# Kernel optimization log

Hardware: AMD Instinct MI355X
Metric: run time of the kernel (lower is better)

## Reference

```python
import math
import jax, jax.numpy as jnp
import numpy as np

DIM = 512; DEPTH = 12; HEADS = 8; DIM_HEAD = 64
INNER = HEADS * DIM_HEAD
FF_INNER = 4 * DIM
B = 8192
NUM_TIMESTEPS = 1000
SCALE = 16.0  # cosine_sim_scale
ROT_DIM = 32  # RotaryEmbedding(dim=min(32, dim_head))
NUM_BUCKETS = 32; MAX_DISTANCE = 128


def layer_norm(x, g, eps=1e-5):
    mean = jnp.mean(x, axis=-1, keepdims=True)
    var = jnp.mean((x - mean) ** 2, axis=-1, keepdims=True)  # unbiased=False
    return (x - mean) * jax.lax.rsqrt(var + eps) * g


def l2norm(t):
    n = jnp.linalg.norm(t, axis=-1, keepdims=True)
    return t / jnp.maximum(n, 1e-12)


def rotary_freqs(n):
    inv = 1.0 / (10000.0 ** (jnp.arange(0, ROT_DIM, 2, dtype=jnp.float32) / ROT_DIM))
    f = jnp.arange(n, dtype=jnp.float32)[:, None] * inv[None, :]  # (n, ROT_DIM//2)
    return jnp.repeat(f, 2, axis=-1)  # (n, ROT_DIM), interleaved pairs


def rotate_half(x):
    x1 = x[..., 0::2]; x2 = x[..., 1::2]
    return jnp.stack((-x2, x1), axis=-1).reshape(x.shape)


def apply_rotary(t, freqs):
    tr, tp = t[..., :ROT_DIM], t[..., ROT_DIM:]
    tr = tr * jnp.cos(freqs) + rotate_half(tr) * jnp.sin(freqs)
    return jnp.concatenate([tr, tp], axis=-1)


def rel_pos_bias(i, j, emb):
    rel = jnp.arange(j)[None, :] - jnp.arange(i)[:, None]
    n = jnp.maximum(-rel, 0)
    max_exact = NUM_BUCKETS // 2
    nf = jnp.maximum(n, 1).astype(jnp.float32)
    val_large = max_exact + (jnp.log(nf / max_exact) / math.log(MAX_DISTANCE / max_exact) * (NUM_BUCKETS - max_exact)).astype(jnp.int32)
    val_large = jnp.minimum(val_large, NUM_BUCKETS - 1)
    bucket = jnp.where(n < max_exact, n, val_large)
    return emb[bucket].transpose(2, 0, 1)  # (h, i, j)


def setup_inputs() -> dict:
    key = jax.random.key(0)
    ks = jax.random.split(key, 13)
    w = 0.02
    return {
        "image_embed": jax.random.normal(ks[0], (B, DIM), jnp.float32),
        "text_embed": jax.random.normal(ks[1], (B, DIM), jnp.float32),
        "timesteps": jax.random.randint(ks[2], (B,), 0, NUM_TIMESTEPS),
        "time_emb_table": jax.random.normal(ks[3], (NUM_TIMESTEPS, DIM)) * w,
        "learned_query": jax.random.normal(ks[4], (DIM,)),
        "rel_emb": jax.random.normal(ks[5], (NUM_BUCKETS, HEADS)) * w,
        "attn_norm_g": jnp.ones((DEPTH, DIM)),
        "Wq": jax.random.normal(ks[6], (DEPTH, DIM, INNER)) * w,
        "Wkv": jax.random.normal(ks[7], (DEPTH, DIM, 2 * DIM_HEAD)) * w,
        "null_kv": jax.random.normal(ks[8], (DEPTH, 2, DIM_HEAD)),
        "Wo": jax.random.normal(ks[9], (DEPTH, INNER, DIM)) * w,
        "attn_out_norm_g": jnp.ones((DEPTH, DIM)),
        "ff_norm_g": jnp.ones((DEPTH, DIM)),
        "Wff1": jax.random.normal(ks[10], (DEPTH, DIM, 2 * FF_INNER)) * w,
        "Wff2": jax.random.normal(ks[11], (DEPTH, FF_INNER, DIM)) * w,
        "final_norm_g": jnp.ones((DIM,)),
        "Wproj": jax.random.normal(ks[12], (DIM, DIM)) * w,
    }


def reference(image_embed, text_embed, timesteps, time_emb_table, learned_query, rel_emb,
              attn_norm_g, Wq, Wkv, null_kv, Wo, attn_out_norm_g,
              ff_norm_g, Wff1, Wff2, final_norm_g, Wproj):
    b = image_embed.shape[0]
    # token sequence: [text_embed, time_embed, image_embed, learned_query] -> (b, 4, dim)
    tokens = jnp.concatenate([
        text_embed[:, None, :],
        time_emb_table[timesteps][:, None, :],
        image_embed[:, None, :],
        jnp.broadcast_to(learned_query, (b, 1, DIM)),
    ], axis=1)
    n = tokens.shape[1]
    bias = rel_pos_bias(n, n + 1, rel_emb)            # (h, n, n+1)
    freqs = rotary_freqs(n)                           # (n, ROT_DIM)
    causal = jnp.triu(jnp.ones((n, n + 1), dtype=bool), k=2)
    neg = -jnp.finfo(jnp.float32).max
    sqrt_scale = math.sqrt(SCALE)

    x = tokens
    for l in range(DEPTH):
        # --- Attention ---
        h = layer_norm(x, attn_norm_g[l])
        q = (h @ Wq[l]).reshape(b, n, HEADS, DIM_HEAD).transpose(0, 2, 1, 3) * SCALE
        kv = h @ Wkv[l]
        k, v = kv[..., :DIM_HEAD], kv[..., DIM_HEAD:]  # single-head kv (b, n, d)
        q = apply_rotary(q, freqs)
        k = apply_rotary(k, freqs)
        nk = jnp.broadcast_to(null_kv[l, 0], (b, 1, DIM_HEAD))
        nv = jnp.broadcast_to(null_kv[l, 1], (b, 1, DIM_HEAD))
        k = jnp.concatenate([nk, k], axis=1)
        v = jnp.concatenate([nv, v], axis=1)
        q = l2norm(q) * sqrt_scale
        k = l2norm(k) * sqrt_scale
        sim = jnp.einsum('bhid,bjd->bhij', q, k) + bias[None]
        sim = jnp.where(causal[None, None], neg, sim)
        attn = jax.nn.softmax(sim.astype(jnp.float32), axis=-1).astype(sim.dtype)
        out = jnp.einsum('bhij,bjd->bhid', attn, v).transpose(0, 2, 1, 3).reshape(b, n, INNER)
        x = x + layer_norm(out @ Wo[l], attn_out_norm_g[l])
        # --- SwiGLU FFN ---
        h = layer_norm(x, ff_norm_g[l])
        hg = h @ Wff1[l]
        a, g = hg[..., :FF_INNER], hg[..., FF_INNER:]
        x = x + (a * jax.nn.silu(g)) @ Wff2[l]

    x = layer_norm(x, final_norm_g) @ Wproj
    return x[:, -1, :]  # predicted image embed from learned query position
```

## Files before the change

### kernel.cpp

```cpp
#include <hip/hip_runtime.h>

typedef __bf16 bf16x8 __attribute__((ext_vector_type(8)));
typedef __bf16 bf16x4 __attribute__((ext_vector_type(4)));
typedef __bf16 bf16x2 __attribute__((ext_vector_type(2)));
typedef float  f32x4  __attribute__((ext_vector_type(4)));
typedef unsigned short u16;

#define BATCH   8192
#define NTOK    4
#define ROWS    (BATCH*NTOK)
#define DIM     512
#define HEADS   8
#define DH      64
#define FFI     2048
#define DEPTH   12
#define LN_EPS  1e-5f

static const size_t OFF_WQKV = 0;
static const size_t SZ_WQKV  = 12ull*640*512*2;
static const size_t OFF_WTO  = OFF_WQKV + SZ_WQKV;
static const size_t SZ_WTO   = 12ull*512*512*2;
static const size_t OFF_WTF1 = OFF_WTO + SZ_WTO;
static const size_t SZ_WTF1  = 12ull*4096*512*2;
static const size_t OFF_WTF2 = OFF_WTF1 + SZ_WTF1;
static const size_t SZ_WTF2  = 12ull*512*2048*2;
static const size_t OFF_WTP  = OFF_WTF2 + SZ_WTF2;
static const size_t SZ_WTP   = 512ull*512*2;
static const size_t OFF_X    = OFF_WTP + SZ_WTP;
static const size_t OFF_H    = OFF_X    + (size_t)ROWS*DIM*4;
static const size_t OFF_QKV  = OFF_H    + (size_t)ROWS*DIM*2;
static const size_t OFF_AO   = OFF_QKV  + (size_t)ROWS*640*2;
static const size_t OFF_FLAG = OFF_AO   + (size_t)ROWS*DIM*2;
static const size_t WS_NEED  = OFF_FLAG + 256;

__device__ __forceinline__ float ldf(const void* p, size_t i, bool b16) {
  return b16 ? (float)((const __bf16*)p)[i] : ((const float*)p)[i];
}

__device__ __forceinline__ void gld_lds16(const void* g, void* l) {
  __builtin_amdgcn_global_load_lds((const __attribute__((address_space(1))) void*)g,
                                   (__attribute__((address_space(3))) void*)l, 16, 0, 0);
}

__device__ __forceinline__ float gsum16(float v) {
  #pragma unroll
  for (int o = 8; o > 0; o >>= 1) v += __shfl_xor(v, o, 64);
  return v;
}

__device__ __forceinline__ void wred2(float& a, float& b) {
  #pragma unroll
  for (int o = 32; o > 0; o >>= 1) { a += __shfl_xor(a, o, 64); b += __shfl_xor(b, o, 64); }
}

__global__ void detect_dtype(const unsigned int* __restrict__ w, int* __restrict__ flag) {
  __shared__ int cnt[4];
  int t = threadIdx.x;
  int c = 0;
  for (int i = t; i < 2048; i += 256) {
    unsigned int v = w[i];
    unsigned int lo = v & 0xFFFFu, hi = v >> 16;
    int elo = (int)((lo >> 7) & 0xFF), ehi = (int)((hi >> 7) & 0xFF);
    bool okl = (lo == 0u) || (elo >= 100 && elo <= 140);
    bool okh = (hi == 0u) || (ehi >= 100 && ehi <= 140);
    if (okl && okh) c++;
  }
  #pragma unroll
  for (int o = 32; o > 0; o >>= 1) c += __shfl_down(c, o, 64);
  if ((t & 63) == 0) cnt[t >> 6] = c;
  __syncthreads();
  if (t == 0) flag[0] = (cnt[0] + cnt[1] + cnt[2] + cnt[3] > 1024) ? 1 : 0;
}

__global__ void transpose_any(const void* __restrict__ in, u16* __restrict__ out,
                              int K, int N, size_t out_zsz, int rowoff, int mode,
                              const int* __restrict__ flag) {
  bool b16 = flag[0] != 0;
  __shared__ u16 tile[32][33];
  size_t iboff = (size_t)blockIdx.z * K * N;
  size_t oboff = (size_t)blockIdx.z * out_zsz;
  int n0 = blockIdx.x * 32, k0 = blockIdx.y * 32;
  int tx = threadIdx.x, ty = threadIdx.y;
  #pragma unroll
  for (int r = 0; r < 4; r++) {
    float v = ldf(in, iboff + (size_t)(k0 + ty*4 + r) * N + n0 + tx, b16);
    __bf16 bv = (__bf16)v;
    tile[ty*4+r][tx] = __builtin_bit_cast(u16, bv);
  }
  __syncthreads();
  int rbase;
  if (mode == 0) rbase = rowoff + n0;
  else {
    int s = (n0 >= 2048) ? 1 : 0;
    int np = n0 - s*2048;
    rbase = (np >> 7)*256 + ((np >> 5) & 3)*64 + s*32;
  }
  #pragma unroll
  for (int r = 0; r < 4; r++)
    out[oboff + (size_t)(rbase + ty*4 + r) * K + k0 + tx] = tile[tx][ty*4+r];
}

__global__ void build_tokens(const void* __restrict__ text, const void* __restrict__ img,
                             const int* __restrict__ ts, const void* __restrict__ table,
                             const void* __restrict__ lq, float* __restrict__ x,
                             const int* __restrict__ flag) {
  bool b16 = flag[0] != 0;
  int b = blockIdx.x, t = threadIdx.x;
  float* xr = x + (size_t)b * NTOK * DIM;
  int tsb = ts[b];
  for (int e = t; e < DIM; e += 256) {
    xr[e]         = ldf(text,  (size_t)b * DIM + e, b16);
    xr[DIM + e]   = ldf(table, (size_t)tsb * DIM + e, b16);
    xr[2*DIM + e] = ldf(img,   (size_t)b * DIM + e, b16);
    xr[3*DIM + e] = ldf(lq,    (size_t)e, b16);
  }
}

__global__ void ln_f32_bf16(const float* __restrict__ x, const void* __restrict__ g, size_t goff,
                            __bf16* __restrict__ out, const int* __restrict__ flag) {
  bool b16 = flag[0] != 0;
  int lane = threadIdx.x & 63;
  int row = blockIdx.x * 4 + (threadIdx.x >> 6);
  const float4* xr = (const float4*)(x + (size_t)row * DIM);
  float4 A4 = xr[lane*2], B4 = xr[lane*2 + 1];
  float v[8] = {A4.x, A4.y, A4.z, A4.w, B4.x, B4.y, B4.z, B4.w};
  float s = 0.f, s2 = 0.f;
  #pragma unroll
  for (int e = 0; e < 8; e++) { s += v[e]; s2 += v[e]*v[e]; }
  wred2(s, s2);
  float mean = s * (1.f/DIM);
  float var  = s2 * (1.f/DIM) - mean*mean;
  float rs = rsqrtf(var + LN_EPS);
  bf16x8 ov;
  #pragma unroll
  for (int e = 0; e < 8; e++)
    ov[e] = (__bf16)((v[e]-mean) * rs * ldf(g, goff + lane*8 + e, b16));
  *(bf16x8*)(out + (size_t)row * DIM + lane*8) = ov;
}

__global__ void ln_add_ln(const __bf16* __restrict__ y,
                          const void* __restrict__ g1, size_t g1off,
                          const void* __restrict__ g2, size_t g2off,
                          float* __restrict__ x, __bf16* __restrict__ h,
                          const int* __restrict__ flag) {
  bool b16 = flag[0] != 0;
  int lane = threadIdx.x & 63;
  int row = blockIdx.x * 4 + (threadIdx.x >> 6);
  bf16x8 y8 = *(const bf16x8*)(y + (size_t)row * DIM + lane*8);
  float yv[8];
  float s = 0.f, s2 = 0.f;
  #pragma unroll
  for (int e = 0; e < 8; e++) { yv[e] = (float)y8[e]; s += yv[e]; s2 += yv[e]*yv[e]; }
  wred2(s, s2);
  float mean = s * (1.f/DIM);
  float var  = s2 * (1.f/DIM) - mean*mean;
  float rs = rsqrtf(var + LN_EPS);
  float4* xr = (float4*)(x + (size_t)row * DIM);
  float4 XA = xr[lane*2], XB = xr[lane*2 + 1];
  float xv[8] = {XA.x, XA.y, XA.z, XA.w, XB.x, XB.y, XB.z, XB.w};
  #pragma unroll
  for (int e = 0; e < 8; e++)
    xv[e] += (yv[e]-mean) * rs * ldf(g1, g1off + lane*8 + e, b16);
  xr[lane*2]     = make_float4(xv[0], xv[1], xv[2], xv[3]);
  xr[lane*2 + 1] = make_float4(xv[4], xv[5], xv[6], xv[7]);
  float t = 0.f, t2 = 0.f;
  #pragma unroll
  for (int e = 0; e < 8; e++) { t += xv[e]; t2 += xv[e]*xv[e]; }
  wred2(t, t2);
  float mean2 = t * (1.f/DIM);
  float var2  = t2 * (1.f/DIM) - mean2*mean2;
  float rs2 = rsqrtf(var2 + LN_EPS);
  bf16x8 hv;
  #pragma unroll
  for (int e = 0; e < 8; e++)
    hv[e] = (__bf16)((xv[e]-mean2) * rs2 * ldf(g2, g2off + lane*8 + e, b16));
  *(bf16x8*)(h + (size_t)row * DIM + lane*8) = hv;
}

__global__ void ln_final(const float* __restrict__ x, const void* __restrict__ g,
                         __bf16* __restrict__ out, const int* __restrict__ flag) {
  bool b16 = flag[0] != 0;
  int lane = threadIdx.x & 63;
  int b = blockIdx.x * 4 + (threadIdx.x >> 6);
  int row = b*NTOK + 3;
  const float4* xr = (const float4*)(x + (size_t)row * DIM);
  float4 A4 = xr[lane*2], B4 = xr[lane*2 + 1];
  float v[8] = {A4.x, A4.y, A4.z, A4.w, B4.x, B4.y, B4.z, B4.w};
  float s = 0.f, s2 = 0.f;
  #pragma unroll
  for (int e = 0; e < 8; e++) { s += v[e]; s2 += v[e]*v[e]; }
  wred2(s, s2);
  float mean = s * (1.f/DIM);
  float var  = s2 * (1.f/DIM) - mean*mean;
  float rs = rsqrtf(var + LN_EPS);
  bf16x8 ov;
  #pragma unroll
  for (int e = 0; e < 8; e++)
    ov[e] = (__bf16)((v[e]-mean) * rs * ldf(g, (size_t)lane*8 + e, b16));
  *(bf16x8*)(out + (size_t)b * DIM + lane*8) = ov;
}

template<int BROWS, int EPI>
__global__ __launch_bounds__(512, 2) void gemm8(
    const __bf16* __restrict__ A, int lda,
    const __bf16* __restrict__ B, int ldb,
    void* __restrict__ Cv, int ldc, int K, const int* __restrict__ flag)
{
  constexpr int UNITS = (BROWS == 256) ? 4 : 3;
  constexpr int WCN   = (BROWS == 256) ? 4 : 2;
  constexpr int M_FR  = (BROWS == 256) ? 8 : 4;
  constexpr int QM    = M_FR / 4;
  __shared__ char ldsmem[2][(256 + BROWS) * 128];

  const int tid = threadIdx.x;
  const int wid = tid >> 6, lane = tid & 63;
  const int wr = wid / WCN, wc = wid % WCN;
  const int lr = lane & 15, lc = lane >> 4;
  const int sr = tid >> 3;
  const int cs = ((tid & 7) ^ (sr & 7)) * 8;
  const int nwg = gridDim.x * gridDim.y;
  const int hw  = blockIdx.y * gridDim.x + blockIdx.x;
  const int nb  = (hw & 7) * (nwg >> 3) + (hw >> 3);
  const int bx = nb % gridDim.x, by = nb / gridDim.x;

  const __bf16* Ab = A + (size_t)by * 256 * lda;
  const __bf16* Bb = B + (size_t)bx * BROWS * ldb;

  f32x4 acc[M_FR][4] = {};
  const int NT = K >> 6;

  char* lds0 = ldsmem[0];
  char* lds1 = ldsmem[1];

  auto stage_unit = [&](int p, int kt, int u) {
    char* base = (p ? lds1 : lds0);
    if (u < 2) {
      const __bf16* s = Ab + (size_t)(u*128 + sr) * lda + kt*64 + cs;
      char* d = base + u*16384 + (wid << 10);
      gld_lds16(s, d);
      gld_lds16(s + (size_t)64 * lda, d + 8192);
    } else {
      const __bf16* s = Bb + (size_t)((u-2)*128 + sr) * ldb + kt*64 + cs;
      char* d = base + 32768 + (u-2)*16384 + (wid << 10);
      gld_lds16(s, d);
      gld_lds16(s + (size_t)64 * ldb, d + 8192);
    }
  };

  #pragma unroll
  for (int u = 0; u < UNITS; u++) stage_unit(0, 0, u);

  const int NIT = NT >> 1;
  for (int i = 0; i < NIT; i++) {
    const int t1 = 2*i + 1;
    const int t2 = (2*i + 2 < NT) ? (2*i + 2) : 0;
    #pragma unroll
    for (int hfl = 0; hfl < 2; hfl++) {
      char* cbase = hfl ? lds1 : lds0;
      const int sp = hfl ^ 1;
      const int st = hfl ? t2 : t1;
      bf16x8 bfr[4][2];
      #pragma unroll
      for (int q = 0; q < 4; q++) {
        if (q < UNITS) stage_unit(sp, st, q);
        if (q == 0) {
          asm volatile("s_waitcnt vmcnt(2)" ::: "memory");
          asm volatile("s_barrier" ::: "memory");
          #pragma unroll
          for (int f = 0; f < 4; f++)
            #pragma unroll
            for (int kk = 0; kk < 2; kk++) {
              int row = wc*64 + f*16 + lr;
              int ch = (kk*4 + lc) ^ (lr & 7);
              bfr[f][kk] = *(const bf16x8*)(cbase + 32768 + row*128 + ch*16);
            }
        }
        bf16x8 afr[QM][2];
        #pragma unroll
        for (int m2 = 0; m2 < QM; m2++)
          #pragma unroll
          for (int kk = 0; kk < 2; kk++) {
            int row = wr*(M_FR*16) + (q*QM + m2)*16 + lr;
            int ch = (kk*4 + lc) ^ (lr & 7);
            afr[m2][kk] = *(const bf16x8*)(cbase + row*128 + ch*16);
          }
        __builtin_amdgcn_s_setprio(1);
        #pragma unroll
        for (int m2 = 0; m2 < QM; m2++)
          #pragma unroll
          for (int n = 0; n < 4; n++)
            #pragma unroll
            for (int kk = 0; kk < 2; kk++)
              acc[q*QM + m2][n] = __builtin_amdgcn_mfma_f32_16x16x32_bf16(
                  afr[m2][kk], bfr[n][kk], acc[q*QM + m2][n], 0, 0, 0);
        __builtin_amdgcn_s_setprio(0);
        asm volatile("s_barrier" ::: "memory");
      }
    }
  }
  asm volatile("s_waitcnt vmcnt(0)" ::: "memory");

  if (EPI == 1) {
    __bf16* Ob = (__bf16*)Cv;
    const int colb = bx*128 + wc*32 + lr;
    const int rowb = by*256 + wr*128 + lc*4;
    #pragma unroll
    for (int m = 0; m < M_FR; m++)
      #pragma unroll
      for (int rr = 0; rr < 4; rr++) {
        size_t ro = (size_t)(rowb + m*16 + rr) * ldc;
        #pragma unroll
        for (int fa = 0; fa < 2; fa++) {
          float a = acc[m][fa][rr], g = acc[m][fa+2][rr];
          Ob[ro + colb + fa*16] = (__bf16)(a * g / (1.f + __expf(-g)));
        }
      }
  } else if (EPI == 2) {
    float* Xf = (float*)Cv;
    const int colb = bx*BROWS + wc*64 + lr;
    const int rowb = by*256 + wr*(M_FR*16) + lc*4;
    #pragma unroll
    for (int m = 0; m < M_FR; m++)
      #pragma unroll
      for (int rr = 0; rr < 4; rr++) {
        size_t ro = (size_t)(rowb + m*16 + rr) * ldc;
        #pragma unroll
        for (int n = 0; n < 4; n++) Xf[ro + colb + n*16] += acc[m][n][rr];
      }
  } else if (EPI == 0) {
    __bf16* Cb = (__bf16*)Cv;
    const int colb = bx*BROWS + wc*64 + lr;
    const int rowb = by*256 + wr*(M_FR*16) + lc*4;
    #pragma unroll
    for (int m = 0; m < M_FR; m++)
      #pragma unroll
      for (int rr = 0; rr < 4; rr++) {
        size_t ro = (size_t)(rowb + m*16 + rr) * ldc;
        #pragma unroll
        for (int n = 0; n < 4; n++) Cb[ro + colb + n*16] = (__bf16)acc[m][n][rr];
      }
  } else {
    bool b16o = flag[0] != 0;
    __bf16* Cb = (__bf16*)Cv;
    float*  Cf = (float*)Cv;
    const int colb = bx*BROWS + wc*64 + lr;
    const int rowb = by*256 + wr*(M_FR*16) + lc*4;
    #pragma unroll
    for (int m = 0; m < M_FR; m++)
      #pragma unroll
      for (int rr = 0; rr < 4; rr++) {
        size_t ro = (size_t)(rowb + m*16 + rr) * ldc;
        #pragma unroll
        for (int n = 0; n < 4; n++) {
          float val = acc[m][n][rr];
          if (b16o) Cb[ro + colb + n*16] = (__bf16)val; else Cf[ro + colb + n*16] = val;
        }
      }
  }
}

__global__ __launch_bounds__(256) void attn_kernel(
    const __bf16* __restrict__ qkv,
    const void* __restrict__ nkv_all, int layer, const void* __restrict__ rel_emb,
    __bf16* __restrict__ ao, const int* __restrict__ flag)
{
  bool b16 = flag[0] != 0;
  const int tid = threadIdx.x;
  const int w = tid >> 6, l = tid & 63;
  const int g = l >> 4, c = l & 15;
  const int bh = blockIdx.x * 16 + w * 4 + g;
  const int b = bh >> 3, h = bh & 7;
  const bool rot = (c < 8);

  const float LN1E4_32 = 9.210340371976184f * (1.f/32.f);
  float inv0 = __expf(-(float)(4*c)     * LN1E4_32);
  float inv1 = __expf(-(float)(4*c + 2) * LN1E4_32);
  float cs0[4], sn0[4], cs1[4], sn1[4];
  #pragma unroll
  for (int t = 0; t < 4; t++) {
    __sincosf((float)t * inv0, &sn0[t], &cs0[t]);
    __sincosf((float)t * inv1, &sn1[t], &cs1[t]);
  }
  float rb[4];
  #pragma unroll
  for (int t = 0; t < 4; t++) rb[t] = ldf(rel_emb, (size_t)t * 8 + h, b16);

  float q[4][4];
  #pragma unroll
  for (int i = 0; i < 4; i++) {
    bf16x4 qv = *(const bf16x4*)(qkv + ((size_t)(b*NTOK + i)) * 640 + h*DH + c*4);
    float v0 = (float)qv[0], v1 = (float)qv[1], v2 = (float)qv[2], v3 = (float)qv[3];
    if (rot) {
      float n0 = v0*cs0[i] - v1*sn0[i], n1 = v1*cs0[i] + v0*sn0[i];
      float n2 = v2*cs1[i] - v3*sn1[i], n3 = v3*cs1[i] + v2*sn1[i];
      v0 = n0; v1 = n1; v2 = n2; v3 = n3;
    }
    q[i][0] = v0; q[i][1] = v1; q[i][2] = v2; q[i][3] = v3;
  }
  #pragma unroll
  for (int i = 0; i < 4; i++) {
    float ss = q[i][0]*q[i][0] + q[i][1]*q[i][1] + q[i][2]*q[i][2] + q[i][3]*q[i][3];
    float r = 1.f / fmaxf(sqrtf(gsum16(ss)), 1e-12f);
    #pragma unroll
    for (int e = 0; e < 4; e++) q[i][e] *= r;
  }

  float kk[5][4], vv[5][4];
  #pragma unroll
  for (int e = 0; e < 4; e++) {
    kk[0][e] = ldf(nkv_all, (size_t)layer*128 + c*4 + e, b16);
    vv[0][e] = ldf(nkv_all, (size_t)layer*128 + 64 + c*4 + e, b16);
  }
  #pragma unroll
  for (int j = 1; j < 5; j++) {
    const __bf16* base = qkv + ((size_t)(b*NTOK + j - 1)) * 640 + 512;
    bf16x4 kv4 = *(const bf16x4*)(base + c*4);
    bf16x4 vv4 = *(const bf16x4*)(base + 64 + c*4);
    float v0 = (float)kv4[0], v1 = (float)kv4[1], v2 = (float)kv4[2], v3 = (float)kv4[3];
    if (rot) {
      int t = j - 1;
      float n0 = v0*cs0[t] - v1*sn0[t], n1 = v1*cs0[t] + v0*sn0[t];
      float n2 = v2*cs1[t] - v3*sn1[t], n3 = v3*cs1[t] + v2*sn1[t];
      v0 = n0; v1 = n1; v2 = n2; v3 = n3;
    }
    kk[j][0] = v0; kk[j][1] = v1; kk[j][2] = v2; kk[j][3] = v3;
    #pragma unroll
    for (int e = 0; e < 4; e++) vv[j][e] = (float)vv4[e];
  }
  #pragma unroll
  for (int j = 0; j < 5; j++) {
    float ss = kk[j][0]*kk[j][0] + kk[j][1]*kk[j][1] + kk[j][2]*kk[j][2] + kk[j][3]*kk[j][3];
    float r = 1.f / fmaxf(sqrtf(gsum16(ss)), 1e-12f);
    #pragma unroll
    for (int e = 0; e < 4; e++) kk[j][e] *= r;
  }

  #pragma unroll
  for (int i = 0; i < 4; i++) {
    float sim[5];
    #pragma unroll
    for (int j = 0; j < 5; j++) {
      if (j > i + 1) break;
      float pp = q[i][0]*kk[j][0] + q[i][1]*kk[j][1] + q[i][2]*kk[j][2] + q[i][3]*kk[j][3];
      sim[j] = 16.f * gsum16(pp) + rb[(i - j > 0) ? (i - j) : 0];
    }
    float m = sim[0];
    #pragma unroll
    for (int j = 1; j < 5; j++) { if (j > i + 1) break; m = fmaxf(m, sim[j]); }
    float Z = 0.f, o0 = 0.f, o1 = 0.f, o2 = 0.f, o3 = 0.f;
    #pragma unroll
    for (int j = 0; j < 5; j++) {
      if (j > i + 1) break;
      float e = __expf(sim[j] - m);
      Z += e;
      o0 += e * vv[j][0]; o1 += e * vv[j][1]; o2 += e * vv[j][2]; o3 += e * vv[j][3];
    }
    float rz = 1.f / Z;
    bf16x4 ov = { (__bf16)(o0*rz), (__bf16)(o1*rz), (__bf16)(o2*rz), (__bf16)(o3*rz) };
    *(bf16x4*)(ao + ((size_t)(b*NTOK + i)) * DIM + h*DH + c*4) = ov;
  }
}

extern "C" void kernel_launch(void* const* d_in, const int* in_sizes, int n_in,
                              void* d_out, int out_size, void* d_ws, size_t ws_size,
                              hipStream_t stream) {
  const void* image_embed     = d_in[0];
  const void* text_embed      = d_in[1];
  const int*  timesteps       = (const int*)d_in[2];
  const void* time_table      = d_in[3];
  const void* learned_query   = d_in[4];
  const void* rel_emb         = d_in[5];
  const void* attn_norm_g     = d_in[6];
  const void* Wq              = d_in[7];
  const void* Wkv             = d_in[8];
  const void* null_kv         = d_in[9];
  const void* Wo              = d_in[10];
  const void* attn_out_norm_g = d_in[11];
  const void* ff_norm_g       = d_in[12];
  const void* Wff1            = d_in[13];
  const void* Wff2            = d_in[14];
  const void* final_norm_g    = d_in[15];
  const void* Wproj           = d_in[16];

  if (ws_size < WS_NEED) return;

  char* ws = (char*)d_ws;
  __bf16* wqkv = (__bf16*)(ws + OFF_WQKV);
  __bf16* wto  = (__bf16*)(ws + OFF_WTO);
  __bf16* wtf1 = (__bf16*)(ws + OFF_WTF1);
  __bf16* wtf2 = (__bf16*)(ws + OFF_WTF2);
  __bf16* wtp  = (__bf16*)(ws + OFF_WTP);
  float*  x    = (float*) (ws + OFF_X);
  __bf16* h    = (__bf16*)(ws + OFF_H);
  __bf16* qkv  = (__bf16*)(ws + OFF_QKV);
  __bf16* ao   = (__bf16*)(ws + OFF_AO);
  __bf16* act  = (__bf16*)(ws + OFF_QKV);
  int*    flag = (int*)   (ws + OFF_FLAG);

  detect_dtype<<<1, 256, 0, stream>>>((const unsigned int*)Wq, flag);

  dim3 tb(32, 8);
  transpose_any<<<dim3(16, 16, 12),  tb, 0, stream>>>(Wq,   (u16*)wqkv, 512,  512,  640ull*512, 0,   0, flag);
  transpose_any<<<dim3(4,  16, 12),  tb, 0, stream>>>(Wkv,  (u16*)wqkv, 512,  128,  640ull*512, 512, 0, flag);
  transpose_any<<<dim3(16, 16, 12),  tb, 0, stream>>>(Wo,   (u16*)wto,  512,  512,  512ull*512, 0,   0, flag);
  transpose_any<<<dim3(128,16, 12),  tb, 0, stream>>>(Wff1, (u16*)wtf1, 512,  4096, 4096ull*512,0,   1, flag);
  transpose_any<<<dim3(16, 64, 12),  tb, 0, stream>>>(Wff2, (u16*)wtf2, 2048, 512,  512ull*2048,0,   0, flag);
  transpose_any<<<dim3(16, 16, 1),   tb, 0, stream>>>(Wproj,(u16*)wtp,  512,  512,  512ull*512, 0,   0, flag);

  build_tokens<<<BATCH, 256, 0, stream>>>(text_embed, image_embed, timesteps, time_table,
                                          learned_query, x, flag);

  for (int l = 0; l < DEPTH; l++) {
    const __bf16* wqkv_l = wqkv + (size_t)l * 640 * 512;
    const __bf16* wto_l  = wto  + (size_t)l * 512 * 512;
    const __bf16* wtf1_l = wtf1 + (size_t)l * 4096 * 512;
    const __bf16* wtf2_l = wtf2 + (size_t)l * 512 * 2048;

    ln_f32_bf16<<<ROWS/4, 256, 0, stream>>>(x, attn_norm_g, (size_t)l*DIM, h, flag);
    gemm8<128,0><<<dim3(5, 128), 512, 0, stream>>>(h, DIM, wqkv_l, 512, qkv, 640, 512, flag);
    attn_kernel<<<BATCH/2, 256, 0, stream>>>(qkv, null_kv, l, rel_emb, ao, flag);
    gemm8<128,0><<<dim3(4, 128), 512, 0, stream>>>(ao, DIM, wto_l, 512, qkv , DIM, 512, flag);
    ln_add_ln<<<ROWS/4, 256, 0, stream>>>(qkv , attn_out_norm_g, (size_t)l*DIM,
                                          ff_norm_g, (size_t)l*DIM, x, h, flag);

    for (int c = 0; c < 2; c++) {
      const __bf16* hc = h + (size_t)c * 16384 * DIM;
      float*        xc = x + (size_t)c * 16384 * DIM;
      gemm8<256,1><<<dim3(16, 64), 512, 0, stream>>>(hc, DIM, wtf1_l, 512, act, FFI, 512, flag);
      gemm8<128,2><<<dim3(4, 64), 512, 0, stream>>>(act, FFI, wtf2_l, FFI, xc, DIM, 2048, flag);
    }
  }

  ln_final<<<BATCH/4, 256, 0, stream>>>(x, final_norm_g, ao , flag);
  gemm8<128,3><<<dim3(4, 32), 512, 0, stream>>>(ao, DIM, wtp, 512, d_out, DIM, 512, flag);
}
```

Measured before the change: 5.412 ms.

## Make FF1 SwiGLU GEMM persistent over four row tiles with cross-tile prefetch

Replaces the FF1 GEMM launch (1024 workgroups) with a new kernel launched as 256 workgroups. Each workgroup keeps one 256-column weight tile and loops over four consecutive 256-row A tiles. During the last K step of one tile it prefetches the first K slice of the next tile, so the pipeline does not drain between tiles. The XCD-aware block remapping in the generic gemm8 is removed at the same time, which changes L2 locality for the other GEMMs. Risks include fewer workgroups to fill the CUs and the SwiGLU epilogue stores no longer overlapping with loads.

```diff
diff --git a/kernel.cpp b/kernel.cpp
--- a/kernel.cpp
+++ b/kernel.cpp
@@ -218,10 +218,7 @@
   const int lr = lane & 15, lc = lane >> 4;
   const int sr = tid >> 3;
   const int cs = ((tid & 7) ^ (sr & 7)) * 8;
-  const int nwg = gridDim.x * gridDim.y;
-  const int hw  = blockIdx.y * gridDim.x + blockIdx.x;
-  const int nb  = (hw & 7) * (nwg >> 3) + (hw >> 3);
-  const int bx = nb % gridDim.x, by = nb / gridDim.x;
+  const int bx = blockIdx.x, by = blockIdx.y;
 
   const __bf16* Ab = A + (size_t)by * 256 * lda;
   const __bf16* Bb = B + (size_t)bx * BROWS * ldb;
@@ -300,22 +297,7 @@
   }
   asm volatile("s_waitcnt vmcnt(0)" ::: "memory");
 
-  if (EPI == 1) {
-    __bf16* Ob = (__bf16*)Cv;
-    const int colb = bx*128 + wc*32 + lr;
-    const int rowb = by*256 + wr*128 + lc*4;
-    #pragma unroll
-    for (int m = 0; m < M_FR; m++)
-      #pragma unroll
-      for (int rr = 0; rr < 4; rr++) {
-        size_t ro = (size_t)(rowb + m*16 + rr) * ldc;
-        #pragma unroll
-        for (int fa = 0; fa < 2; fa++) {
-          float a = acc[m][fa][rr], g = acc[m][fa+2][rr];
-          Ob[ro + colb + fa*16] = (__bf16)(a * g / (1.f + __expf(-g)));
-        }
-      }
-  } else if (EPI == 2) {
+  if (EPI == 2) {
     float* Xf = (float*)Cv;
     const int colb = bx*BROWS + wc*64 + lr;
     const int rowb = by*256 + wr*(M_FR*16) + lc*4;
@@ -357,6 +339,122 @@
         }
       }
   }
+}
+
+__global__ __launch_bounds__(512, 2) void gemm8p(
+    const __bf16* __restrict__ A, int lda,
+    const __bf16* __restrict__ B, int ldb,
+    __bf16* __restrict__ Out, int ldc, int K)
+{
+  constexpr int M_FR = 8;
+  constexpr int QM   = 2;
+  __shared__ char ldsmem[2][512 * 128];
+
+  const int tid = threadIdx.x;
+  const int wid = tid >> 6, lane = tid & 63;
+  const int wr = wid >> 2, wc = wid & 3;
+  const int lr = lane & 15, lc = lane >> 4;
+  const int sr = tid >> 3;
+  const int cs = ((tid & 7) ^ (sr & 7)) * 8;
+  const int bx = blockIdx.x & 15;
+  const int by0 = (blockIdx.x >> 4) * 4;
+
+  const __bf16* Bb = B + (size_t)bx * 256 * ldb;
+  const int NT = K >> 6;
+  const int NIT = NT >> 1;
+
+  char* lds0 = ldsmem[0];
+  char* lds1 = ldsmem[1];
+
+  auto stage_unit = [&](const __bf16* Ab, int p, int kt, int u) {
+    char* base = (p ? lds1 : lds0);
+    if (u < 2) {
+      const __bf16* s = Ab + (size_t)(u*128 + sr) * lda + kt*64 + cs;
+      char* d = base + u*16384 + (wid << 10);
+      gld_lds16(s, d);
+      gld_lds16(s + (size_t)64 * lda, d + 8192);
+    } else {
+      const __bf16* s = Bb + (size_t)((u-2)*128 + sr) * ldb + kt*64 + cs;
+      char* d = base + 32768 + (u-2)*16384 + (wid << 10);
+      gld_lds16(s, d);
+      gld_lds16(s + (size_t)64 * ldb, d + 8192);
+    }
+  };
+
+  const __bf16* Ab = A + (size_t)by0 * 256 * lda;
+  #pragma unroll
+  for (int u = 0; u < 4; u++) stage_unit(Ab, 0, 0, u);
+
+  for (int j = 0; j < 4; j++) {
+    const __bf16* Ab_nxt = A + (size_t)(by0 + ((j+1) & 3)) * 256 * lda;
+    f32x4 acc[M_FR][4] = {};
+    for (int i = 0; i < NIT; i++) {
+      const int t1 = 2*i + 1;
+      const bool last = (2*i + 2 >= NT);
+      const int t2 = last ? 0 : (2*i + 2);
+      #pragma unroll
+      for (int hfl = 0; hfl < 2; hfl++) {
+        char* cbase = hfl ? lds1 : lds0;
+        const int sp = hfl ^ 1;
+        const int st = hfl ? t2 : t1;
+        const __bf16* Asrc = (hfl && last) ? Ab_nxt : Ab;
+        bf16x8 bfr[4][2];
+        #pragma unroll
+        for (int q = 0; q < 4; q++) {
+          stage_unit(Asrc, sp, st, q);
+          if (q == 0) {
+            asm volatile("s_waitcnt vmcnt(2)" ::: "memory");
+            asm volatile("s_barrier" ::: "memory");
+            #pragma unroll
+            for (int f = 0; f < 4; f++)
+              #pragma unroll
+              for (int kk = 0; kk < 2; kk++) {
+                int row = wc*64 + f*16 + lr;
+                int ch = (kk*4 + lc) ^ (lr & 7);
+                bfr[f][kk] = *(const bf16x8*)(cbase + 32768 + row*128 + ch*16);
+              }
+          }
+          bf16x8 afr[QM][2];
+          #pragma unroll
+          for (int m2 = 0; m2 < QM; m2++)
+            #pragma unroll
+            for (int kk = 0; kk < 2; kk++) {
+              int row = wr*128 + (q*QM + m2)*16 + lr;
+              int ch = (kk*4 + lc) ^ (lr & 7);
+              afr[m2][kk] = *(const bf16x8*)(cbase + row*128 + ch*16);
+            }
+          __builtin_amdgcn_s_setprio(1);
+          #pragma unroll
+          for (int m2 = 0; m2 < QM; m2++)
+            #pragma unroll
+            for (int n = 0; n < 4; n++)
+              #pragma unroll
+              for (int kk = 0; kk < 2; kk++)
+                acc[q*QM + m2][n] = __builtin_amdgcn_mfma_f32_16x16x32_bf16(
+                    afr[m2][kk], bfr[n][kk], acc[q*QM + m2][n], 0, 0, 0);
+          __builtin_amdgcn_s_setprio(0);
+          asm volatile("s_barrier" ::: "memory");
+        }
+      }
+    }
+    {
+      const int colb = bx*128 + wc*32 + lr;
+      const int rowb = (by0 + j)*256 + wr*128 + lc*4;
+      #pragma unroll
+      for (int m = 0; m < M_FR; m++)
+        #pragma unroll
+        for (int rr = 0; rr < 4; rr++) {
+          size_t ro = (size_t)(rowb + m*16 + rr) * ldc;
+          #pragma unroll
+          for (int fa = 0; fa < 2; fa++) {
+            float a = acc[m][fa][rr], g = acc[m][fa+2][rr];
+            Out[ro + colb + fa*16] = (__bf16)(a * g / (1.f + __expf(-g)));
+          }
+        }
+    }
+    Ab = Ab_nxt;
+  }
+  asm volatile("s_waitcnt vmcnt(0)" ::: "memory");
 }
 
 __global__ __launch_bounds__(256) void attn_kernel(
@@ -526,7 +624,7 @@
     for (int c = 0; c < 2; c++) {
       const __bf16* hc = h + (size_t)c * 16384 * DIM;
       float*        xc = x + (size_t)c * 16384 * DIM;
-      gemm8<256,1><<<dim3(16, 64), 512, 0, stream>>>(hc, DIM, wtf1_l, 512, act, FFI, 512, flag);
+      gemm8p<<<256, 512, 0, stream>>>(hc, DIM, wtf1_l, 512, act, FFI, 512);
       gemm8<128,2><<<dim3(4, 64), 512, 0, stream>>>(act, FFI, wtf2_l, FFI, xc, DIM, 2048, flag);
     }
   }
```

After: 5.683 ms. 1.05x slower.
